# Optimization experiments

Measured on AMD Instinct MI355X. Metric: run time of the kernel, lower is better.

Reference implementation:

```python
import jax, jax.numpy as jnp
import numpy as np

SINKHORN_ITERS = 20
EPS = 1e-6


def sinkhorn(M, n_iter=SINKHORN_ITERS, eps=EPS):
    # Project (n, n) logits onto the Birkhoff polytope (doubly stochastic).
    A = jnp.exp(M - jnp.max(M, axis=(-2, -1), keepdims=True))
    for _ in range(n_iter):
        A = A / (A.sum(axis=-1, keepdims=True) + eps)
        A = A / (A.sum(axis=-2, keepdims=True) + eps)
    return A


def setup_inputs() -> dict:
    key = jax.random.key(0)
    k1, k2, k3, k4 = jax.random.split(key, 4)
    B, S, D, E = 4, 4096, 4096, 4
    return {
        "x": jax.random.normal(k1, (B, S, D), dtype=jnp.float32),
        "H_res_logits": jax.random.normal(k2, (E, E), dtype=jnp.float32),
        "H_pre_logits": jax.random.normal(k3, (E, D), dtype=jnp.float32),
        "H_post_logits": jax.random.normal(k4, (E, D), dtype=jnp.float32),
    }


def reference(x, H_res_logits, H_pre_logits, H_post_logits):
    # MHCLayer forward with layer=None (residual routing only), sinkhorn projection.
    H_res = sinkhorn(H_res_logits)                      # (E, E) doubly stochastic
    H_pre = jax.nn.softmax(H_pre_logits, axis=-1)       # (E, D)
    H_post = jax.nn.softmax(H_post_logits, axis=-1)     # (E, D)

    # x_pre = (x.unsqueeze(-2) * H_pre).sum(-1)  ==  x @ H_pre^T
    x_pre = jnp.einsum("bsd,ed->bse", x, H_pre)         # (B, S, E)
    out_exp = x_pre @ H_res                             # (B, S, E)
    # out = (out_exp.unsqueeze(-1) * H_post).sum(-2)  ==  out_exp @ H_post
    out = jnp.einsum("bse,ed->bsd", out_exp, H_post)    # (B, S, D)
    return out
```

## Files before the change

### kernel.cpp

```cpp
#include <hip/hip_runtime.h>
#include <math.h>

#define E 4
#define TPB 256
#define RPB 8
#define NWAVES (TPB / 64)
#define SINKHORN_ITERS 20
#define SINKHORN_EPS 1e-6f

typedef float f4 __attribute__((ext_vector_type(4)));

__global__ __launch_bounds__(TPB) void prep_kernel(
    const float* __restrict__ Hres_l,
    const float* __restrict__ Hpre_l,
    const float* __restrict__ Hpost_l,
    float* __restrict__ ws_pre,
    float* __restrict__ ws_post2,
    int D)
{
    __shared__ float sHres[E * E];
    __shared__ float smx[2 * E], ssm[2 * E];
    const int t = threadIdx.x;
    const int wave = t >> 6;
    const int lane = t & 63;
    const int D4 = D >> 2;

    if (wave == 0) {
        float a = (lane < E * E) ? Hres_l[lane] : -1e30f;
        float m = a;
#pragma unroll
        for (int off = 1; off < 16; off <<= 1)
            m = fmaxf(m, __shfl_xor(m, off, 16));
        a = expf(a - m);
        for (int it = 0; it < SINKHORN_ITERS; ++it) {
            float rs = a;
            rs += __shfl_xor(rs, 1, 4);
            rs += __shfl_xor(rs, 2, 4);
            a /= (rs + SINKHORN_EPS);
            float cs = a;
            cs += __shfl_xor(cs, 4, 16);
            cs += __shfl_xor(cs, 8, 16);
            a /= (cs + SINKHORN_EPS);
        }
        if (lane < E * E) sHres[lane] = a;
    }

    for (int pi = 0; pi < 2; ++pi) {
        const int p = wave * 2 + pi;
        const int mat = p >> 2, e = p & 3;
        const f4* rowp = (const f4*)((mat ? Hpost_l : Hpre_l) + (size_t)e * D);
        float m = -1e30f;
        for (int i = lane; i < D4; i += 64) {
            f4 v = rowp[i];
            m = fmaxf(fmaxf(fmaxf(m, v.x), v.y), fmaxf(v.z, v.w));
        }
#pragma unroll
        for (int off = 1; off < 64; off <<= 1)
            m = fmaxf(m, __shfl_xor(m, off, 64));
        float s = 0.f;
        for (int i = lane; i < D4; i += 64) {
            f4 v = rowp[i];
            s += expf(v.x - m) + expf(v.y - m) + expf(v.z - m) + expf(v.w - m);
        }
#pragma unroll
        for (int off = 1; off < 64; off <<= 1)
            s += __shfl_xor(s, off, 64);
        if (lane == 0) { smx[p] = m; ssm[p] = s; }
    }
    __syncthreads();

    float hres[E * E];
#pragma unroll
    for (int i = 0; i < E * E; ++i) hres[i] = sHres[i];
    float mpre[E], spre[E], mpost[E], spost[E];
#pragma unroll
    for (int e = 0; e < E; ++e) {
        mpre[e] = smx[e];      spre[e] = 1.f / ssm[e];
        mpost[e] = smx[E + e]; spost[e] = 1.f / ssm[E + e];
    }

    const f4* pre_l4  = (const f4*)Hpre_l;
    const f4* post_l4 = (const f4*)Hpost_l;
    f4* wpre4  = (f4*)ws_pre;
    f4* wpost4 = (f4*)ws_post2;
    for (int i = t; i < D4; i += TPB) {
        f4 postv[E];
#pragma unroll
        for (int e = 0; e < E; ++e) {
            f4 v = pre_l4[(size_t)e * D4 + i];
            f4 o;
            o.x = expf(v.x - mpre[e]) * spre[e];
            o.y = expf(v.y - mpre[e]) * spre[e];
            o.z = expf(v.z - mpre[e]) * spre[e];
            o.w = expf(v.w - mpre[e]) * spre[e];
            wpre4[(size_t)e * D4 + i] = o;
            f4 w = post_l4[(size_t)e * D4 + i];
            postv[e].x = expf(w.x - mpost[e]) * spost[e];
            postv[e].y = expf(w.y - mpost[e]) * spost[e];
            postv[e].z = expf(w.z - mpost[e]) * spost[e];
            postv[e].w = expf(w.w - mpost[e]) * spost[e];
        }
#pragma unroll
        for (int ep = 0; ep < E; ++ep) {
            f4 o = hres[ep * E + 0] * postv[0] + hres[ep * E + 1] * postv[1] +
                   hres[ep * E + 2] * postv[2] + hres[ep * E + 3] * postv[3];
            wpost4[(size_t)ep * D4 + i] = o;
        }
    }
}

__global__ __launch_bounds__(TPB) void xpre_kernel(
    const f4* __restrict__ x4,
    const f4* __restrict__ pre4,
    float* __restrict__ xpre,
    int D4, int chunks)
{
    __shared__ float wred[NWAVES][RPB][E];
    const int t = threadIdx.x;
    const int wave = t >> 6;
    const long row0 = (long)blockIdx.x * RPB;

    float part[RPB][E];
#pragma unroll
    for (int r = 0; r < RPB; ++r)
#pragma unroll
        for (int e = 0; e < E; ++e) part[r][e] = 0.f;

    for (int k = 0; k < chunks; ++k) {
        const int d4 = k * TPB + t;
        f4 hp[E];
#pragma unroll
        for (int e = 0; e < E; ++e) hp[e] = pre4[(size_t)e * D4 + d4];
#pragma unroll
        for (int r = 0; r < RPB; ++r) {
            f4 xv = __builtin_nontemporal_load(&x4[(row0 + r) * D4 + d4]);
#pragma unroll
            for (int e = 0; e < E; ++e)
                part[r][e] += xv.x * hp[e].x + xv.y * hp[e].y +
                              xv.z * hp[e].z + xv.w * hp[e].w;
        }
    }

#pragma unroll
    for (int r = 0; r < RPB; ++r)
#pragma unroll
        for (int e = 0; e < E; ++e) {
            float v = part[r][e];
#pragma unroll
            for (int off = 1; off < 64; off <<= 1) v += __shfl_xor(v, off, 64);
            if ((t & 63) == 0) wred[wave][r][e] = v;
        }
    __syncthreads();

    if (t < RPB * E) {
        const int r = t >> 2, e = t & 3;
        float v = 0.f;
#pragma unroll
        for (int w = 0; w < NWAVES; ++w) v += wred[w][r][e];
        xpre[(row0 + r) * E + e] = v;
    }
}

__global__ __launch_bounds__(TPB) void out_kernel(
    const float* __restrict__ xpre,
    const f4* __restrict__ post4,
    f4* __restrict__ out4,
    int D4, int chunks)
{
    __shared__ float sxp[RPB * E];
    const int t = threadIdx.x;
    const long row0 = (long)blockIdx.x * RPB;

    if (t < RPB * E) sxp[t] = xpre[row0 * E + t];
    __syncthreads();

    float xp[RPB][E];
#pragma unroll
    for (int r = 0; r < RPB; ++r)
#pragma unroll
        for (int e = 0; e < E; ++e) xp[r][e] = sxp[r * E + e];

    for (int k = 0; k < chunks; ++k) {
        const int d4 = k * TPB + t;
        f4 hq[E];
#pragma unroll
        for (int e = 0; e < E; ++e) hq[e] = post4[(size_t)e * D4 + d4];
#pragma unroll
        for (int r = 0; r < RPB; ++r) {
            f4 o = xp[r][0] * hq[0] + xp[r][1] * hq[1] +
                   xp[r][2] * hq[2] + xp[r][3] * hq[3];
            __builtin_nontemporal_store(o, &out4[(row0 + r) * D4 + d4]);
        }
    }
}

extern "C" void kernel_launch(void* const* d_in, const int* in_sizes, int n_in,
                              void* d_out, int out_size, void* d_ws, size_t ws_size,
                              hipStream_t stream) {
    const float* x     = (const float*)d_in[0];
    const float* Hres  = (const float*)d_in[1];
    const float* Hpre  = (const float*)d_in[2];
    const float* Hpost = (const float*)d_in[3];
    float* out = (float*)d_out;

    const int D = in_sizes[2] / E;
    const long rows = (long)in_sizes[0] / D;

    float* ws_pre   = (float*)d_ws;
    float* ws_post2 = ws_pre + (size_t)E * D;
    float* ws_xpre  = ws_post2 + (size_t)E * D;

    prep_kernel<<<1, TPB, 0, stream>>>(Hres, Hpre, Hpost, ws_pre, ws_post2, D);

    const int D4 = D / 4;
    const int chunks = D4 / TPB;
    const int grid = (int)(rows / RPB);

    xpre_kernel<<<grid, TPB, 0, stream>>>((const f4*)x, (const f4*)ws_pre,
                                          ws_xpre, D4, chunks);
    out_kernel<<<grid, TPB, 0, stream>>>(ws_xpre, (const f4*)ws_post2,
                                         (f4*)out, D4, chunks);
}
```

Measured before the change: 131.2 us.

## Fuse x_pre and output kernels, split prep into parallel stats and write kernels

Merges the projection-reduction kernel and the output-expansion kernel into one kernel, so the per-row x_pre values stay in registers and shared memory and never round-trip through global memory. This also drops one launch. The single-block prep kernel is split into a stats kernel and a grid-wide write kernel, spreading the softmax and post-mix writes across many blocks. It also fully unrolls the chunk loops through a compile-time template and replaces the nontemporal loads and stores with ordinary ones, which may change how x and out interact with the cache.

Measured after the change: 145.7 us. 11.1% more time.

```diff
diff --git a/kernel.cpp b/kernel.cpp
--- a/kernel.cpp
+++ b/kernel.cpp
@@ -10,20 +10,17 @@
 
 typedef float f4 __attribute__((ext_vector_type(4)));
 
-__global__ __launch_bounds__(TPB) void prep_kernel(
+
+__global__ __launch_bounds__(TPB) void prep_stats(
     const float* __restrict__ Hres_l,
     const float* __restrict__ Hpre_l,
     const float* __restrict__ Hpost_l,
-    float* __restrict__ ws_pre,
-    float* __restrict__ ws_post2,
-    int D)
+    float* __restrict__ ws_small,
+    int D4)
 {
-    __shared__ float sHres[E * E];
-    __shared__ float smx[2 * E], ssm[2 * E];
     const int t = threadIdx.x;
     const int wave = t >> 6;
     const int lane = t & 63;
-    const int D4 = D >> 2;
 
     if (wave == 0) {
         float a = (lane < E * E) ? Hres_l[lane] : -1e30f;
@@ -42,13 +39,13 @@
             cs += __shfl_xor(cs, 8, 16);
             a /= (cs + SINKHORN_EPS);
         }
-        if (lane < E * E) sHres[lane] = a;
+        if (lane < E * E) ws_small[lane] = a;
     }
 
     for (int pi = 0; pi < 2; ++pi) {
         const int p = wave * 2 + pi;
         const int mat = p >> 2, e = p & 3;
-        const f4* rowp = (const f4*)((mat ? Hpost_l : Hpre_l) + (size_t)e * D);
+        const f4* rowp = (const f4*)((mat ? Hpost_l : Hpre_l) + (size_t)e * D4 * 4);
         float m = -1e30f;
         for (int i = lane; i < D4; i += 64) {
             f4 v = rowp[i];
@@ -65,60 +62,70 @@
 #pragma unroll
         for (int off = 1; off < 64; off <<= 1)
             s += __shfl_xor(s, off, 64);
-        if (lane == 0) { smx[p] = m; ssm[p] = s; }
-    }
-    __syncthreads();
+        if (lane == 0) { ws_small[16 + p] = m; ws_small[24 + p] = s; }
+    }
+}
+
+__global__ __launch_bounds__(TPB) void prep_write(
+    const float* __restrict__ Hpre_l,
+    const float* __restrict__ Hpost_l,
+    const float* __restrict__ ws_small,
+    f4* __restrict__ wpre4,
+    f4* __restrict__ wpost4,
+    int D4)
+{
+    const int i = blockIdx.x * TPB + threadIdx.x;
+    if (i >= D4) return;
 
     float hres[E * E];
 #pragma unroll
-    for (int i = 0; i < E * E; ++i) hres[i] = sHres[i];
+    for (int k = 0; k < E * E; ++k) hres[k] = ws_small[k];
     float mpre[E], spre[E], mpost[E], spost[E];
 #pragma unroll
     for (int e = 0; e < E; ++e) {
-        mpre[e] = smx[e];      spre[e] = 1.f / ssm[e];
-        mpost[e] = smx[E + e]; spost[e] = 1.f / ssm[E + e];
+        mpre[e]  = ws_small[16 + e];     spre[e]  = 1.f / ws_small[24 + e];
+        mpost[e] = ws_small[16 + E + e]; spost[e] = 1.f / ws_small[24 + E + e];
     }
 
     const f4* pre_l4  = (const f4*)Hpre_l;
     const f4* post_l4 = (const f4*)Hpost_l;
-    f4* wpre4  = (f4*)ws_pre;
-    f4* wpost4 = (f4*)ws_post2;
-    for (int i = t; i < D4; i += TPB) {
-        f4 postv[E];
-#pragma unroll
-        for (int e = 0; e < E; ++e) {
-            f4 v = pre_l4[(size_t)e * D4 + i];
-            f4 o;
-            o.x = expf(v.x - mpre[e]) * spre[e];
-            o.y = expf(v.y - mpre[e]) * spre[e];
-            o.z = expf(v.z - mpre[e]) * spre[e];
-            o.w = expf(v.w - mpre[e]) * spre[e];
-            wpre4[(size_t)e * D4 + i] = o;
-            f4 w = post_l4[(size_t)e * D4 + i];
-            postv[e].x = expf(w.x - mpost[e]) * spost[e];
-            postv[e].y = expf(w.y - mpost[e]) * spost[e];
-            postv[e].z = expf(w.z - mpost[e]) * spost[e];
-            postv[e].w = expf(w.w - mpost[e]) * spost[e];
-        }
-#pragma unroll
-        for (int ep = 0; ep < E; ++ep) {
-            f4 o = hres[ep * E + 0] * postv[0] + hres[ep * E + 1] * postv[1] +
-                   hres[ep * E + 2] * postv[2] + hres[ep * E + 3] * postv[3];
-            wpost4[(size_t)ep * D4 + i] = o;
-        }
-    }
-}
-
-__global__ __launch_bounds__(TPB) void xpre_kernel(
+    f4 postv[E];
+#pragma unroll
+    for (int e = 0; e < E; ++e) {
+        f4 v = pre_l4[(size_t)e * D4 + i];
+        f4 o;
+        o.x = expf(v.x - mpre[e]) * spre[e];
+        o.y = expf(v.y - mpre[e]) * spre[e];
+        o.z = expf(v.z - mpre[e]) * spre[e];
+        o.w = expf(v.w - mpre[e]) * spre[e];
+        wpre4[(size_t)e * D4 + i] = o;
+        f4 w = post_l4[(size_t)e * D4 + i];
+        postv[e].x = expf(w.x - mpost[e]) * spost[e];
+        postv[e].y = expf(w.y - mpost[e]) * spost[e];
+        postv[e].z = expf(w.z - mpost[e]) * spost[e];
+        postv[e].w = expf(w.w - mpost[e]) * spost[e];
+    }
+#pragma unroll
+    for (int ep = 0; ep < E; ++ep) {
+        f4 o = hres[ep * E + 0] * postv[0] + hres[ep * E + 1] * postv[1] +
+               hres[ep * E + 2] * postv[2] + hres[ep * E + 3] * postv[3];
+        wpost4[(size_t)ep * D4 + i] = o;
+    }
+}
+
+template <int CT>
+__global__ __launch_bounds__(TPB) void mhc_main(
     const f4* __restrict__ x4,
     const f4* __restrict__ pre4,
-    float* __restrict__ xpre,
-    int D4, int chunks)
+    const f4* __restrict__ post4,
+    f4* __restrict__ out4,
+    int D4, int chunks_rt)
 {
     __shared__ float wred[NWAVES][RPB][E];
     const int t = threadIdx.x;
     const int wave = t >> 6;
     const long row0 = (long)blockIdx.x * RPB;
+    const int chunks = CT ? CT : chunks_rt;
 
     float part[RPB][E];
 #pragma unroll
@@ -126,6 +133,7 @@
 #pragma unroll
         for (int e = 0; e < E; ++e) part[r][e] = 0.f;
 
+#pragma unroll
     for (int k = 0; k < chunks; ++k) {
         const int d4 = k * TPB + t;
         f4 hp[E];
@@ -133,7 +141,7 @@
         for (int e = 0; e < E; ++e) hp[e] = pre4[(size_t)e * D4 + d4];
 #pragma unroll
         for (int r = 0; r < RPB; ++r) {
-            f4 xv = __builtin_nontemporal_load(&x4[(row0 + r) * D4 + d4]);
+            f4 xv = x4[(row0 + r) * D4 + d4];
 #pragma unroll
             for (int e = 0; e < E; ++e)
                 part[r][e] += xv.x * hp[e].x + xv.y * hp[e].y +
@@ -152,34 +160,18 @@
         }
     __syncthreads();
 
-    if (t < RPB * E) {
-        const int r = t >> 2, e = t & 3;
-        float v = 0.f;
-#pragma unroll
-        for (int w = 0; w < NWAVES; ++w) v += wred[w][r][e];
-        xpre[(row0 + r) * E + e] = v;
-    }
-}
-
-__global__ __launch_bounds__(TPB) void out_kernel(
-    const float* __restrict__ xpre,
-    const f4* __restrict__ post4,
-    f4* __restrict__ out4,
-    int D4, int chunks)
-{
-    __shared__ float sxp[RPB * E];
-    const int t = threadIdx.x;
-    const long row0 = (long)blockIdx.x * RPB;
-
-    if (t < RPB * E) sxp[t] = xpre[row0 * E + t];
-    __syncthreads();
-
     float xp[RPB][E];
 #pragma unroll
     for (int r = 0; r < RPB; ++r)
 #pragma unroll
-        for (int e = 0; e < E; ++e) xp[r][e] = sxp[r * E + e];
-
+        for (int e = 0; e < E; ++e) {
+            float v = 0.f;
+#pragma unroll
+            for (int w = 0; w < NWAVES; ++w) v += wred[w][r][e];
+            xp[r][e] = v;
+        }
+
+#pragma unroll
     for (int k = 0; k < chunks; ++k) {
         const int d4 = k * TPB + t;
         f4 hq[E];
@@ -189,7 +181,7 @@
         for (int r = 0; r < RPB; ++r) {
             f4 o = xp[r][0] * hq[0] + xp[r][1] * hq[1] +
                    xp[r][2] * hq[2] + xp[r][3] * hq[3];
-            __builtin_nontemporal_store(o, &out4[(row0 + r) * D4 + d4]);
+            out4[(row0 + r) * D4 + d4] = o;
         }
     }
 }
@@ -205,19 +197,25 @@
 
     const int D = in_sizes[2] / E;
     const long rows = (long)in_sizes[0] / D;
+    const int D4 = D / 4;
+    const int chunks = D4 / TPB;
 
     float* ws_pre   = (float*)d_ws;
     float* ws_post2 = ws_pre + (size_t)E * D;
-    float* ws_xpre  = ws_post2 + (size_t)E * D;
-
-    prep_kernel<<<1, TPB, 0, stream>>>(Hres, Hpre, Hpost, ws_pre, ws_post2, D);
-
-    const int D4 = D / 4;
-    const int chunks = D4 / TPB;
+    float* ws_small = ws_post2 + (size_t)E * D;
+
+    prep_stats<<<1, TPB, 0, stream>>>(Hres, Hpre, Hpost, ws_small, D4);
+    prep_write<<<(D4 + TPB - 1) / TPB, TPB, 0, stream>>>(
+        Hpre, Hpost, ws_small, (f4*)ws_pre, (f4*)ws_post2, D4);
+
     const int grid = (int)(rows / RPB);
-
-    xpre_kernel<<<grid, TPB, 0, stream>>>((const f4*)x, (const f4*)ws_pre,
-                                          ws_xpre, D4, chunks);
-    out_kernel<<<grid, TPB, 0, stream>>>(ws_xpre, (const f4*)ws_post2,
-                                         (f4*)out, D4, chunks);
-}
+    if (chunks == 4 && D4 % TPB == 0) {
+        mhc_main<4><<<grid, TPB, 0, stream>>>((const f4*)x, (const f4*)ws_pre,
+                                              (const f4*)ws_post2, (f4*)out,
+                                              D4, chunks);
+    } else {
+        mhc_main<0><<<grid, TPB, 0, stream>>>((const f4*)x, (const f4*)ws_pre,
+                                              (const f4*)ws_post2, (f4*)out,
+                                              D4, chunks);
+    }
+}
```
